# Kernel tuning notes

Measured on AMD Instinct MI355X. Metric: run time of the kernel, lower is better.

Reference implementation:

```python
import jax, jax.numpy as jnp
import numpy as np

N = 100000   # nodes
E = 1600000  # directed edges
HID = 64


def gat_conv(x, src, dst, W, a_src, a_dst, b, heads, out_ch):
    """PyG-style GATConv (add_self_loops=True, negative_slope=0.2, concat)."""
    n = x.shape[0]
    h = (x @ W).reshape(n, heads, out_ch)              # [N,H,C]
    loop = jnp.arange(n, dtype=src.dtype)
    s = jnp.concatenate([src, loop])                   # self loops appended
    d = jnp.concatenate([dst, loop])
    alpha_src = jnp.sum(h * a_src, axis=-1)            # [N,H]
    alpha_dst = jnp.sum(h * a_dst, axis=-1)            # [N,H]
    alpha = jax.nn.leaky_relu(alpha_src[s] + alpha_dst[d], 0.2)  # [E+N,H]
    # segment softmax over incoming edges of each destination node
    amax = jax.ops.segment_max(alpha, d, num_segments=n)
    alpha = jnp.exp(alpha - amax[d])
    asum = jax.ops.segment_sum(alpha, d, num_segments=n)
    alpha = alpha / (asum[d] + 1e-16)
    msg = h[s] * alpha[:, :, None]                     # [E+N,H,C]
    out = jax.ops.segment_sum(msg, d, num_segments=n)  # [N,H,C]
    return out.reshape(n, heads * out_ch) + b


def setup_inputs() -> dict:
    key = jax.random.key(0)
    ks = jax.random.split(key, 22)
    rn = lambda k, shp, s=0.1: (jax.random.normal(k, shp, jnp.float32) * s)
    inp = {
        "x": jax.random.normal(ks[0], (N, 2), jnp.float32),
        "edge_index": jax.random.randint(ks[1], (2, E), 0, N, dtype=jnp.int32),
        "edge_attr": jax.random.normal(ks[2], (E, 2), jnp.float32),
        # node encoder
        "enc_W": rn(ks[3], (2, HID)), "enc_b": rn(ks[4], (HID,)),
        # gat1: heads=4, out=16
        "g1_W": rn(ks[5], (HID, HID)), "g1_as": rn(ks[6], (4, 16)),
        "g1_ad": rn(ks[7], (4, 16)), "g1_b": rn(ks[8], (HID,)),
        # gat2: heads=1, out=64
        "g2_W": rn(ks[9], (HID, HID)), "g2_as": rn(ks[10], (1, HID)),
        "g2_ad": rn(ks[11], (1, HID)), "g2_b": rn(ks[12], (HID,)),
        # node head
        "no_W1": rn(ks[13], (HID, HID)), "no_b1": rn(ks[14], (HID,)),
        "no_W2": rn(ks[15], (HID, 2)), "no_b2": rn(ks[16], (2,)),
        # edge head: in = 2*HID + 2 = 130
        "eo_W1": rn(ks[17], (2 * HID + 2, HID)), "eo_b1": rn(ks[18], (HID,)),
        "eo_W2": rn(ks[19], (HID, 1)), "eo_b2": rn(ks[20], (1,)),
    }
    return inp


def reference(x, edge_index, edge_attr, enc_W, enc_b,
              g1_W, g1_as, g1_ad, g1_b,
              g2_W, g2_as, g2_ad, g2_b,
              no_W1, no_b1, no_W2, no_b2,
              eo_W1, eo_b1, eo_W2, eo_b2):
    src, dst = edge_index[0], edge_index[1]
    h = x @ enc_W + enc_b                                    # node encoder (dropout = eval identity)
    h = jax.nn.elu(gat_conv(h, src, dst, g1_W, g1_as, g1_ad, g1_b, 4, 16))
    h = gat_conv(h, src, dst, g2_W, g2_as, g2_ad, g2_b, 1, HID)
    e_in = jnp.concatenate([h[src], h[dst], edge_attr], axis=-1)  # [E,130]
    node_pred = jnp.tanh(jax.nn.leaky_relu(h @ no_W1 + no_b1, 0.01) @ no_W2 + no_b2)
    edge_pred = jnp.tanh(jax.nn.leaky_relu(e_in @ eo_W1 + eo_b1, 0.01) @ eo_W2 + eo_b2)[:, 0]
    return edge_pred, node_pred
```

## Files before the change

kernel.cpp:

```cpp
#include <hip/hip_runtime.h>
#include <hip/hip_fp16.h>
#include <math.h>


typedef _Float16 half8_t __attribute__((ext_vector_type(8)));
typedef _Float16 half4_t __attribute__((ext_vector_type(4)));
typedef float floatx4 __attribute__((ext_vector_type(4)));

__global__ void k_scatter(const int* __restrict__ src, const int* __restrict__ dst,
                          int E, int NB, int cap, int* cursor,
                          unsigned int* __restrict__ ebuf,
                          const float* __restrict__ encW, const float* __restrict__ encb,
                          const float* __restrict__ g1W, float* __restrict__ Mc){
  __shared__ int hist[800];
  __shared__ int base[800];
  int t = threadIdx.x;
  if (blockIdx.x == 0 && t < 64){
    float m0 = 0.f, m1 = 0.f, cc = 0.f;
    for (int k = 0; k < 64; ++k){
      float g = g1W[k * 64 + t];
      m0 = fmaf(encW[k], g, m0);
      m1 = fmaf(encW[64 + k], g, m1);
      cc = fmaf(encb[k], g, cc);
    }
    Mc[t] = m0; Mc[64 + t] = m1; Mc[128 + t] = cc;
  }
  for (int i = t; i < NB; i += 256) hist[i] = 0;
  __syncthreads();
  int cbase = blockIdx.x * 2048;
  int sv[8], bk[8], dl[8], rk[8];
  #pragma unroll
  for (int i = 0; i < 8; ++i){
    int e = cbase + i * 256 + t;
    if (e < E){
      int d = dst[e];
      sv[i] = src[e]; bk[i] = d >> 7; dl[i] = d & 127;
      rk[i] = atomicAdd(&hist[bk[i]], 1);
    } else bk[i] = -1;
  }
  __syncthreads();
  for (int i = t; i < NB; i += 256){
    int c = hist[i];
    base[i] = (c > 0) ? (i * cap + atomicAdd(&cursor[i], c)) : 0;
  }
  __syncthreads();
  #pragma unroll
  for (int i = 0; i < 8; ++i){
    if (bk[i] >= 0){
      int p = base[bk[i]] + rk[i];
      if (p < (bk[i] + 1) * cap)
        ebuf[p] = (unsigned)sv[i] | ((unsigned)dl[i] << 17);
    }
  }
}

__global__ void k_bucket_build(const int* __restrict__ cursor, int cap, int N,
                               unsigned int* ebuf, int* __restrict__ rstart,
                               int* __restrict__ rend,
                               const float* __restrict__ as4,
                               const float* __restrict__ ad4,
                               half4_t* __restrict__ palpha4){
  __shared__ unsigned int ent[2700];
  __shared__ unsigned short rank[2700];
  __shared__ int cnts[128];
  __shared__ int aux[128];
  int b = blockIdx.x, t = threadIdx.x;
  int base = b * cap;
  int cnt = cursor[b];
  if (cnt > cap) cnt = cap;
  for (int i = t; i < cnt; i += 256) ent[i] = ebuf[base + i];
  if (t < 128) cnts[t] = 0;
  __syncthreads();
  for (int i = t; i < cnt; i += 256)
    rank[i] = (unsigned short)atomicAdd(&cnts[ent[i] >> 17], 1);
  __syncthreads();
  int v = 0;
  if (t < 128){ v = cnts[t]; aux[t] = v; }
  __syncthreads();
  for (int off = 1; off < 128; off <<= 1){
    int x = 0;
    if (t < 128 && t >= off) x = aux[t - off];
    __syncthreads();
    if (t < 128) aux[t] += x;
    __syncthreads();
  }
  if (t < 128){
    int incl = aux[t];
    int node = (b << 7) + t;
    if (node < N){ rstart[node] = base + incl - v; rend[node] = base + incl; }
    cnts[t] = incl - v;
  }
  __syncthreads();
  for (int i = t; i < cnt; i += 256){
    unsigned int en = ent[i];
    int dl = en >> 17;
    int s = en & 0x1FFFFu;
    int pos = cnts[dl] + (int)rank[i];
    ebuf[base + pos] = en;
    int d = (b << 7) + dl;
    float4 sv = ((const float4*)as4)[s];
    float4 dv = ((const float4*)ad4)[d];
    float a0 = sv.x + dv.x, a1 = sv.y + dv.y, a2 = sv.z + dv.z, a3 = sv.w + dv.w;
    a0 = a0 > 0.f ? a0 : 0.2f * a0;
    a1 = a1 > 0.f ? a1 : 0.2f * a1;
    a2 = a2 > 0.f ? a2 : 0.2f * a2;
    a3 = a3 > 0.f ? a3 : 0.2f * a3;
    half4_t pv = {(_Float16)__expf(a0), (_Float16)__expf(a1),
                  (_Float16)__expf(a2), (_Float16)__expf(a3)};
    palpha4[base + pos] = pv;
  }
}

__global__ void k_palpha1(const int* __restrict__ cursor, int cap,
                          const unsigned int* __restrict__ ebuf,
                          const float* __restrict__ as, const float* __restrict__ ad,
                          _Float16* __restrict__ palpha1){
  int blk = blockIdx.x;
  int b = blk >> 2, part = blk & 3;
  int base = b * cap;
  int cnt = cursor[b];
  if (cnt > cap) cnt = cap;
  for (int i = part * 256 + threadIdx.x; i < cnt; i += 1024){
    unsigned int en = ebuf[base + i];
    int s = en & 0x1FFFFu;
    int d = (b << 7) + (en >> 17);
    float a = as[s] + ad[d];
    a = a > 0.f ? a : 0.2f * a;
    palpha1[base + i] = (_Float16)__expf(a);
  }
}

__global__ void k_fuse1(const float* __restrict__ x, const float* __restrict__ Mc,
                        const float* __restrict__ a_s, const float* __restrict__ a_d,
                        __half* __restrict__ hw, float* __restrict__ alpha_s,
                        float* __restrict__ alpha_d, int n){
  int idx = blockIdx.x * blockDim.x + threadIdx.x;
  if (idx >= n * 64) return;
  int node = idx >> 6, j = idx & 63;
  float acc = fmaf(x[node * 2 + 0], Mc[j], fmaf(x[node * 2 + 1], Mc[64 + j], Mc[128 + j]));
  hw[idx] = __float2half(acc);
  float ps = acc * a_s[j];
  float pd = acc * a_d[j];
  #pragma unroll
  for (int off = 1; off < 16; off <<= 1){
    ps += __shfl_xor(ps, off);
    pd += __shfl_xor(pd, off);
  }
  if ((j & 15) == 0){
    int h = j >> 4;
    alpha_s[node * 4 + h] = ps;
    alpha_d[node * 4 + h] = pd;
  }
}

__global__ __launch_bounds__(256) void k_hw_mfma(
    const __half* __restrict__ hin, const float* __restrict__ W,
    const float* __restrict__ a_s, const float* __restrict__ a_d,
    __half* __restrict__ hw, float* __restrict__ alpha_s,
    float* __restrict__ alpha_d, int n){
  __shared__ float redS[4][16];
  __shared__ float redD[4][16];
  int t = threadIdx.x;
  int lane = t & 63, wave = t >> 6;
  int l15 = lane & 15, quad = lane >> 4;
  int ch = wave * 16 + l15;
  half8_t b0, b1;
  #pragma unroll
  for (int j = 0; j < 8; ++j){
    b0[j] = (_Float16)W[(quad * 8 + j) * 64 + ch];
    b1[j] = (_Float16)W[(quad * 8 + j + 32) * 64 + ch];
  }
  float asv = a_s[ch], adv = a_d[ch];
  int base = blockIdx.x * 64;
  for (int it = 0; it < 4; ++it){
    int tb = base + it * 16;
    if (tb >= n) break;
    int arn = tb + l15; if (arn >= n) arn = n - 1;
    const __half* arow = hin + (size_t)arn * 64 + quad * 8;
    half8_t a0 = *(const half8_t*)arow;
    half8_t a1 = *(const half8_t*)(arow + 32);
    floatx4 acc = {0.f, 0.f, 0.f, 0.f};
    acc = __builtin_amdgcn_mfma_f32_16x16x32_f16(a0, b0, acc, 0, 0, 0);
    acc = __builtin_amdgcn_mfma_f32_16x16x32_f16(a1, b1, acc, 0, 0, 0);
    float ps[4], pd[4];
    #pragma unroll
    for (int r = 0; r < 4; ++r){
      int node = tb + quad * 4 + r;
      if (node < n) hw[(size_t)node * 64 + ch] = __float2half(acc[r]);
      ps[r] = acc[r] * asv;
      pd[r] = acc[r] * adv;
      #pragma unroll
      for (int off = 1; off < 16; off <<= 1){
        ps[r] += __shfl_xor(ps[r], off);
        pd[r] += __shfl_xor(pd[r], off);
      }
    }
    if (l15 == 0){
      #pragma unroll
      for (int r = 0; r < 4; ++r){
        redS[wave][quad * 4 + r] = ps[r];
        redD[wave][quad * 4 + r] = pd[r];
      }
    }
    __syncthreads();
    if (t < 16 && tb + t < n){
      alpha_s[tb + t] = redS[0][t] + redS[1][t] + redS[2][t] + redS[3][t];
      alpha_d[tb + t] = redD[0][t] + redD[1][t] + redD[2][t] + redD[3][t];
    }
    __syncthreads();
  }
}

template<int H, bool ELU_ACT>
__global__ void k_agg(const __half* __restrict__ hw, const _Float16* __restrict__ palpha,
                      const float* __restrict__ alpha_s, const float* __restrict__ alpha_d,
                      const int* __restrict__ rstart, const int* __restrict__ rend,
                      const unsigned int* __restrict__ ebuf,
                      const float* __restrict__ bias, __half* __restrict__ hout, int n){
  int node = (blockIdx.x * blockDim.x + threadIdx.x) >> 6;
  int lane = threadIdx.x & 63;
  int g = lane >> 3, jj = lane & 7;
  if (node >= n) return;
  int hidx = (jj * H) >> 3;
  int start = rstart[node], end = rend[node];
  float acc[8] = {0.f,0.f,0.f,0.f,0.f,0.f,0.f,0.f};
  float psum = 0.f;
  if (g == 0){
    float a = alpha_s[node * H + hidx] + alpha_d[node * H + hidx];
    a = a > 0.f ? a : 0.2f * a;
    float p = __expf(a);
    psum = p;
    float4 rv = *(const float4*)(hw + (size_t)node * 64 + jj * 8);
    const __half2* hp = (const __half2*)&rv;
    #pragma unroll
    for (int k = 0; k < 4; ++k){
      float2 f = __half22float2(hp[k]);
      acc[2 * k] = p * f.x; acc[2 * k + 1] = p * f.y;
    }
  }
  int i = start + g;
  for (; i + 8 < end; i += 16){
    unsigned int e0 = ebuf[i], e1 = ebuf[i + 8];
    int s0 = e0 & 0x1FFFF, s1 = e1 & 0x1FFFF;
    float p0 = (float)palpha[(size_t)i * H + hidx];
    float p1 = (float)palpha[(size_t)(i + 8) * H + hidx];
    float4 r0 = *(const float4*)(hw + (size_t)s0 * 64 + jj * 8);
    float4 r1 = *(const float4*)(hw + (size_t)s1 * 64 + jj * 8);
    const __half2* h0 = (const __half2*)&r0;
    const __half2* h1 = (const __half2*)&r1;
    psum += p0 + p1;
    #pragma unroll
    for (int k = 0; k < 4; ++k){
      float2 f0 = __half22float2(h0[k]);
      float2 f1 = __half22float2(h1[k]);
      acc[2 * k]     = fmaf(p0, f0.x, fmaf(p1, f1.x, acc[2 * k]));
      acc[2 * k + 1] = fmaf(p0, f0.y, fmaf(p1, f1.y, acc[2 * k + 1]));
    }
  }
  if (i < end){
    unsigned int en = ebuf[i];
    int s = en & 0x1FFFF;
    float p = (float)palpha[(size_t)i * H + hidx];
    float4 rv = *(const float4*)(hw + (size_t)s * 64 + jj * 8);
    const __half2* hp = (const __half2*)&rv;
    psum += p;
    #pragma unroll
    for (int k = 0; k < 4; ++k){
      float2 f = __half22float2(hp[k]);
      acc[2 * k]     = fmaf(p, f.x, acc[2 * k]);
      acc[2 * k + 1] = fmaf(p, f.y, acc[2 * k + 1]);
    }
  }
  #pragma unroll
  for (int off = 8; off < 64; off <<= 1){
    psum += __shfl_xor(psum, off);
    #pragma unroll
    for (int k = 0; k < 8; ++k) acc[k] += __shfl_xor(acc[k], off);
  }
  if (g == 0){
    float inv = 1.f / (psum + 1e-16f);
    float4 bv0 = ((const float4*)bias)[2 * jj];
    float4 bv1 = ((const float4*)bias)[2 * jj + 1];
    float o[8];
    o[0] = fmaf(acc[0], inv, bv0.x); o[1] = fmaf(acc[1], inv, bv0.y);
    o[2] = fmaf(acc[2], inv, bv0.z); o[3] = fmaf(acc[3], inv, bv0.w);
    o[4] = fmaf(acc[4], inv, bv1.x); o[5] = fmaf(acc[5], inv, bv1.y);
    o[6] = fmaf(acc[6], inv, bv1.z); o[7] = fmaf(acc[7], inv, bv1.w);
    if (ELU_ACT){
      #pragma unroll
      for (int k = 0; k < 8; ++k) o[k] = o[k] > 0.f ? o[k] : (__expf(o[k]) - 1.f);
    }
    half8_t hv;
    #pragma unroll
    for (int k = 0; k < 8; ++k) hv[k] = (_Float16)o[k];
    *(half8_t*)(hout + (size_t)node * 64 + jj * 8) = hv;
  }
}

__global__ __launch_bounds__(256) void k_heads_mfma(
    const __half* __restrict__ h, const float* __restrict__ eoW1,
    const float* __restrict__ noW1, const float* __restrict__ nob1,
    const float* __restrict__ noW2, const float* __restrict__ nob2,
    __half* __restrict__ P1, __half* __restrict__ P2,
    float* __restrict__ outN, int n){
  __shared__ float redP[4][16][2];
  int t = threadIdx.x;
  int lane = t & 63, wave = t >> 6;
  int l15 = lane & 15, quad = lane >> 4;
  int ch = wave * 16 + l15;
  half8_t bP1a, bP1b, bP2a, bP2b, bNa, bNb;
  #pragma unroll
  for (int j = 0; j < 8; ++j){
    int k0 = quad * 8 + j, k1 = k0 + 32;
    bP1a[j] = (_Float16)eoW1[k0 * 64 + ch];
    bP1b[j] = (_Float16)eoW1[k1 * 64 + ch];
    bP2a[j] = (_Float16)eoW1[(k0 + 64) * 64 + ch];
    bP2b[j] = (_Float16)eoW1[(k1 + 64) * 64 + ch];
    bNa[j]  = (_Float16)noW1[k0 * 64 + ch];
    bNb[j]  = (_Float16)noW1[k1 * 64 + ch];
  }
  float b1v = nob1[ch];
  float w20 = noW2[ch * 2 + 0], w21 = noW2[ch * 2 + 1];
  float b20 = nob2[0], b21 = nob2[1];
  int base = blockIdx.x * 64;
  for (int it = 0; it < 4; ++it){
    int tb = base + it * 16;
    if (tb >= n) break;
    int arn = tb + l15; if (arn >= n) arn = n - 1;
    const __half* arow = h + (size_t)arn * 64 + quad * 8;
    half8_t a0 = *(const half8_t*)arow;
    half8_t a1 = *(const half8_t*)(arow + 32);
    floatx4 ac1 = {0.f,0.f,0.f,0.f}, ac2 = {0.f,0.f,0.f,0.f}, acN = {0.f,0.f,0.f,0.f};
    ac1 = __builtin_amdgcn_mfma_f32_16x16x32_f16(a0, bP1a, ac1, 0, 0, 0);
    ac1 = __builtin_amdgcn_mfma_f32_16x16x32_f16(a1, bP1b, ac1, 0, 0, 0);
    ac2 = __builtin_amdgcn_mfma_f32_16x16x32_f16(a0, bP2a, ac2, 0, 0, 0);
    ac2 = __builtin_amdgcn_mfma_f32_16x16x32_f16(a1, bP2b, ac2, 0, 0, 0);
    acN = __builtin_amdgcn_mfma_f32_16x16x32_f16(a0, bNa, acN, 0, 0, 0);
    acN = __builtin_amdgcn_mfma_f32_16x16x32_f16(a1, bNb, acN, 0, 0, 0);
    float p0[4], p1[4];
    #pragma unroll
    for (int r = 0; r < 4; ++r){
      int node = tb + quad * 4 + r;
      if (node < n){
        P1[(size_t)node * 64 + ch] = __float2half(ac1[r]);
        P2[(size_t)node * 64 + ch] = __float2half(ac2[r]);
      }
      float v = acN[r] + b1v;
      v = v > 0.f ? v : 0.01f * v;
      p0[r] = v * w20;
      p1[r] = v * w21;
      #pragma unroll
      for (int off = 1; off < 16; off <<= 1){
        p0[r] += __shfl_xor(p0[r], off);
        p1[r] += __shfl_xor(p1[r], off);
      }
    }
    if (l15 == 0){
      #pragma unroll
      for (int r = 0; r < 4; ++r){
        redP[wave][quad * 4 + r][0] = p0[r];
        redP[wave][quad * 4 + r][1] = p1[r];
      }
    }
    __syncthreads();
    if (t < 16 && tb + t < n){
      float s0 = redP[0][t][0] + redP[1][t][0] + redP[2][t][0] + redP[3][t][0];
      float s1 = redP[0][t][1] + redP[1][t][1] + redP[2][t][1] + redP[3][t][1];
      outN[(size_t)(tb + t) * 2 + 0] = tanhf(s0 + b20);
      outN[(size_t)(tb + t) * 2 + 1] = tanhf(s1 + b21);
    }
    __syncthreads();
  }
}

__global__ void k_edge_head(const __half* __restrict__ P1h, const __half* __restrict__ P2h,
                            const int* __restrict__ src, const int* __restrict__ dst,
                            const float* __restrict__ eattr, const float* __restrict__ eoW1,
                            const float* __restrict__ b1, const float* __restrict__ W2,
                            const float* __restrict__ b2, float* __restrict__ out, int E){
  int lane = threadIdx.x & 63;
  int jj = lane & 7, q = lane >> 3;
  int wid = (blockIdx.x * blockDim.x + threadIdx.x) >> 6;
  int nw = (gridDim.x * blockDim.x) >> 6;

  const float4* rAq = (const float4*)(eoW1 + 8192);
  const float4* rBq = (const float4*)(eoW1 + 8256);
  const float4* b1q = (const float4*)b1;
  const float4* w2q = (const float4*)W2;
  float4 tA0 = rAq[2 * jj], tA1 = rAq[2 * jj + 1];
  float4 tB0 = rBq[2 * jj], tB1 = rBq[2 * jj + 1];
  float4 tb0 = b1q[2 * jj], tb1 = b1q[2 * jj + 1];
  float4 tw0 = w2q[2 * jj], tw1 = w2q[2 * jj + 1];
  float ra[8] = {tA0.x, tA0.y, tA0.z, tA0.w, tA1.x, tA1.y, tA1.z, tA1.w};
  float rb[8] = {tB0.x, tB0.y, tB0.z, tB0.w, tB1.x, tB1.y, tB1.z, tB1.w};
  float bb[8] = {tb0.x, tb0.y, tb0.z, tb0.w, tb1.x, tb1.y, tb1.z, tb1.w};
  float w2[8] = {tw0.x, tw0.y, tw0.z, tw0.w, tw1.x, tw1.y, tw1.z, tw1.w};
  float b2v = b2[0];

  const float4* P1q = (const float4*)P1h;
  const float4* P2q = (const float4*)P2h;
  const float2* eav = (const float2*)eattr;

  int groups = (E + 15) >> 4;
  for (int g = wid; g < groups; g += nw){
    int e0 = g * 16 + q, e1 = e0 + 8;
    bool act0 = (e0 < E), act1 = (e1 < E);
    float p0 = 0.f, p1 = 0.f;
    if (act0){
      int s = src[e0], d = dst[e0];
      float2 ea = eav[e0];
      float4 g1 = P1q[(size_t)s * 8 + jj];
      float4 g2 = P2q[(size_t)d * 8 + jj];
      const __half2* h1 = (const __half2*)&g1;
      const __half2* h2 = (const __half2*)&g2;
      #pragma unroll
      for (int k = 0; k < 4; ++k){
        float2 u = __half22float2(h1[k]);
        float2 w = __half22float2(h2[k]);
        float ta = u.x + w.x + bb[2 * k];
        float tb = u.y + w.y + bb[2 * k + 1];
        ta = fmaf(ea.x, ra[2 * k], fmaf(ea.y, rb[2 * k], ta));
        tb = fmaf(ea.x, ra[2 * k + 1], fmaf(ea.y, rb[2 * k + 1], tb));
        ta = ta > 0.f ? ta : 0.01f * ta;
        tb = tb > 0.f ? tb : 0.01f * tb;
        p0 = fmaf(ta, w2[2 * k], fmaf(tb, w2[2 * k + 1], p0));
      }
    }
    if (act1){
      int s = src[e1], d = dst[e1];
      float2 ea = eav[e1];
      float4 g1 = P1q[(size_t)s * 8 + jj];
      float4 g2 = P2q[(size_t)d * 8 + jj];
      const __half2* h1 = (const __half2*)&g1;
      const __half2* h2 = (const __half2*)&g2;
      #pragma unroll
      for (int k = 0; k < 4; ++k){
        float2 u = __half22float2(h1[k]);
        float2 w = __half22float2(h2[k]);
        float ta = u.x + w.x + bb[2 * k];
        float tb = u.y + w.y + bb[2 * k + 1];
        ta = fmaf(ea.x, ra[2 * k], fmaf(ea.y, rb[2 * k], ta));
        tb = fmaf(ea.x, ra[2 * k + 1], fmaf(ea.y, rb[2 * k + 1], tb));
        ta = ta > 0.f ? ta : 0.01f * ta;
        tb = tb > 0.f ? tb : 0.01f * tb;
        p1 = fmaf(ta, w2[2 * k], fmaf(tb, w2[2 * k + 1], p1));
      }
    }
    #pragma unroll
    for (int off = 1; off < 8; off <<= 1){
      p0 += __shfl_xor(p0, off);
      p1 += __shfl_xor(p1, off);
    }
    if (jj == 0){
      if (act0) out[e0] = tanhf(p0 + b2v);
      if (act1) out[e1] = tanhf(p1 + b2v);
    }
  }
}

extern "C" void kernel_launch(void* const* d_in, const int* in_sizes, int n_in,
                              void* d_out, int out_size, void* d_ws, size_t ws_size,
                              hipStream_t stream){
  const float* x    = (const float*)d_in[0];
  const int*   eidx = (const int*)  d_in[1];
  const float* ea   = (const float*)d_in[2];
  const float* encW = (const float*)d_in[3];
  const float* encb = (const float*)d_in[4];
  const float* g1W  = (const float*)d_in[5];
  const float* g1as = (const float*)d_in[6];
  const float* g1ad = (const float*)d_in[7];
  const float* g1b  = (const float*)d_in[8];
  const float* g2W  = (const float*)d_in[9];
  const float* g2as = (const float*)d_in[10];
  const float* g2ad = (const float*)d_in[11];
  const float* g2b  = (const float*)d_in[12];
  const float* noW1 = (const float*)d_in[13];
  const float* nob1 = (const float*)d_in[14];
  const float* noW2 = (const float*)d_in[15];
  const float* nob2 = (const float*)d_in[16];
  const float* eoW1 = (const float*)d_in[17];
  const float* eob1 = (const float*)d_in[18];
  const float* eoW2 = (const float*)d_in[19];
  const float* eob2 = (const float*)d_in[20];

  const int N = in_sizes[0] / 2;
  const int E = in_sizes[1] / 2;
  const int* src = eidx;
  const int* dst = eidx + E;

  const int NB = (N + 127) >> 7;
  int avg = (E + NB - 1) / NB;
  int cap = avg + avg / 4 + 64;
  if (cap > 2700) cap = 2700;

  char* ws = (char*)d_ws;
  size_t off = 0;
  auto alloc = [&](size_t bytes) -> void* {
    void* p = ws + off;
    off = (off + bytes + 255) & ~(size_t)255;
    return p;
  };
  __half* bufA  = (__half*)alloc((size_t)N * 64 * 2);
  __half* bufH  = (__half*)alloc((size_t)N * 64 * 2);
  __half* P1h   = (__half*)alloc((size_t)N * 64 * 2);
  __half* P2h   = (__half*)alloc((size_t)N * 64 * 2);
  float*  as    = (float*) alloc((size_t)N * 4 * 4);
  float*  ad    = (float*) alloc((size_t)N * 4 * 4);
  int* rstart   = (int*)   alloc((size_t)N * 4);
  int* rend     = (int*)   alloc((size_t)N * 4);
  unsigned int* ebuf = (unsigned int*)alloc((size_t)NB * cap * 4);
  _Float16* palphaB = (_Float16*)alloc((size_t)NB * cap * 8);
  int* cursor   = (int*)   alloc((size_t)NB * 4);
  float* Mc     = (float*) alloc(192 * 4);

  hipMemsetAsync(cursor, 0, (size_t)NB * 4, stream);
  k_scatter<<<(E + 2047) / 2048, 256, 0, stream>>>(src, dst, E, NB, cap, cursor, ebuf,
                                                   encW, encb, g1W, Mc);
  k_fuse1<<<(N * 64 + 255) / 256, 256, 0, stream>>>(x, Mc, g1as, g1ad, bufH, as, ad, N);
  k_bucket_build<<<NB, 256, 0, stream>>>(cursor, cap, N, ebuf, rstart, rend,
                                         as, ad, (half4_t*)palphaB);
  k_agg<4, true><<<(N + 3) / 4, 256, 0, stream>>>(bufH, palphaB, as, ad,
                                                  rstart, rend, ebuf, g1b, bufA, N);
  k_hw_mfma<<<(N + 63) / 64, 256, 0, stream>>>(bufA, g2W, g2as, g2ad, bufH, as, ad, N);
  k_palpha1<<<NB * 4, 256, 0, stream>>>(cursor, cap, ebuf, as, ad, palphaB);
  k_agg<1, false><<<(N + 3) / 4, 256, 0, stream>>>(bufH, palphaB, as, ad,
                                                   rstart, rend, ebuf, g2b, bufA, N);
  float* out = (float*)d_out;
  k_heads_mfma<<<(N + 63) / 64, 256, 0, stream>>>(bufA, eoW1, noW1, nob1, noW2, nob2,
                                                  P1h, P2h, out + E, N);
  k_edge_head<<<2048, 256, 0, stream>>>(P1h, P2h, src, dst, ea,
                                        eoW1, eob1, eoW2, eob2, out, E);
}
```

Measured before the change: 387.4 us.

## Fuse node encoder into scatter kernel and inline layer-2 attention in aggregation

Merges the first-layer projection (k_fuse1) into the edge scatter kernel via a grid-stride loop, with every block recomputing the small folded weight matrix into shared memory. It also drops the k_palpha1 pass by computing layer-2 edge attention weights on the fly inside the aggregation kernel from alpha_s/alpha_d. The goal is fewer launches and no write-then-read of the per-edge palpha buffer. In exchange each block repeats the 64x64 fold, and each edge in layer 2 needs an extra gather of alpha_s plus an exp.

New measurement: 378.2 us. 2.4% less time.

```diff
diff --git a/kernel.cpp b/kernel.cpp
--- a/kernel.cpp
+++ b/kernel.cpp
@@ -7,15 +7,20 @@
 typedef _Float16 half4_t __attribute__((ext_vector_type(4)));
 typedef float floatx4 __attribute__((ext_vector_type(4)));
 
-__global__ void k_scatter(const int* __restrict__ src, const int* __restrict__ dst,
-                          int E, int NB, int cap, int* cursor,
-                          unsigned int* __restrict__ ebuf,
-                          const float* __restrict__ encW, const float* __restrict__ encb,
-                          const float* __restrict__ g1W, float* __restrict__ Mc){
+__global__ void k_scatter_fuse(const int* __restrict__ src, const int* __restrict__ dst,
+                               int E, int NB, int cap, int* cursor,
+                               unsigned int* __restrict__ ebuf,
+                               const float* __restrict__ x,
+                               const float* __restrict__ encW, const float* __restrict__ encb,
+                               const float* __restrict__ g1W,
+                               const float* __restrict__ g1as, const float* __restrict__ g1ad,
+                               __half* __restrict__ hw, float* __restrict__ alpha_s,
+                               float* __restrict__ alpha_d, int n){
   __shared__ int hist[800];
   __shared__ int base[800];
+  __shared__ float McS[192];
   int t = threadIdx.x;
-  if (blockIdx.x == 0 && t < 64){
+  if (t < 64){
     float m0 = 0.f, m1 = 0.f, cc = 0.f;
     for (int k = 0; k < 64; ++k){
       float g = g1W[k * 64 + t];
@@ -23,7 +28,7 @@
       m1 = fmaf(encW[64 + k], g, m1);
       cc = fmaf(encb[k], g, cc);
     }
-    Mc[t] = m0; Mc[64 + t] = m1; Mc[128 + t] = cc;
+    McS[t] = m0; McS[64 + t] = m1; McS[128 + t] = cc;
   }
   for (int i = t; i < NB; i += 256) hist[i] = 0;
   __syncthreads();
@@ -50,6 +55,26 @@
       int p = base[bk[i]] + rk[i];
       if (p < (bk[i] + 1) * cap)
         ebuf[p] = (unsigned)sv[i] | ((unsigned)dl[i] << 17);
+    }
+  }
+  int total = n * 64;
+  int lane = t & 63;
+  for (int idx = blockIdx.x * 256 + t; idx < total; idx += gridDim.x * 256){
+    int node = idx >> 6;
+    float acc = fmaf(x[node * 2 + 0], McS[lane],
+                fmaf(x[node * 2 + 1], McS[64 + lane], McS[128 + lane]));
+    hw[idx] = __float2half(acc);
+    float ps = acc * g1as[lane];
+    float pd = acc * g1ad[lane];
+    #pragma unroll
+    for (int off = 1; off < 16; off <<= 1){
+      ps += __shfl_xor(ps, off);
+      pd += __shfl_xor(pd, off);
+    }
+    if ((lane & 15) == 0){
+      int h = lane >> 4;
+      alpha_s[node * 4 + h] = ps;
+      alpha_d[node * 4 + h] = pd;
     }
   }
 }
@@ -111,48 +136,6 @@
   }
 }
 
-__global__ void k_palpha1(const int* __restrict__ cursor, int cap,
-                          const unsigned int* __restrict__ ebuf,
-                          const float* __restrict__ as, const float* __restrict__ ad,
-                          _Float16* __restrict__ palpha1){
-  int blk = blockIdx.x;
-  int b = blk >> 2, part = blk & 3;
-  int base = b * cap;
-  int cnt = cursor[b];
-  if (cnt > cap) cnt = cap;
-  for (int i = part * 256 + threadIdx.x; i < cnt; i += 1024){
-    unsigned int en = ebuf[base + i];
-    int s = en & 0x1FFFFu;
-    int d = (b << 7) + (en >> 17);
-    float a = as[s] + ad[d];
-    a = a > 0.f ? a : 0.2f * a;
-    palpha1[base + i] = (_Float16)__expf(a);
-  }
-}
-
-__global__ void k_fuse1(const float* __restrict__ x, const float* __restrict__ Mc,
-                        const float* __restrict__ a_s, const float* __restrict__ a_d,
-                        __half* __restrict__ hw, float* __restrict__ alpha_s,
-                        float* __restrict__ alpha_d, int n){
-  int idx = blockIdx.x * blockDim.x + threadIdx.x;
-  if (idx >= n * 64) return;
-  int node = idx >> 6, j = idx & 63;
-  float acc = fmaf(x[node * 2 + 0], Mc[j], fmaf(x[node * 2 + 1], Mc[64 + j], Mc[128 + j]));
-  hw[idx] = __float2half(acc);
-  float ps = acc * a_s[j];
-  float pd = acc * a_d[j];
-  #pragma unroll
-  for (int off = 1; off < 16; off <<= 1){
-    ps += __shfl_xor(ps, off);
-    pd += __shfl_xor(pd, off);
-  }
-  if ((j & 15) == 0){
-    int h = j >> 4;
-    alpha_s[node * 4 + h] = ps;
-    alpha_d[node * 4 + h] = pd;
-  }
-}
-
 __global__ __launch_bounds__(256) void k_hw_mfma(
     const __half* __restrict__ hin, const float* __restrict__ W,
     const float* __restrict__ a_s, const float* __restrict__ a_d,
@@ -211,7 +194,7 @@
   }
 }
 
-template<int H, bool ELU_ACT>
+template<int H, bool ELU_ACT, bool INLINE_A>
 __global__ void k_agg(const __half* __restrict__ hw, const _Float16* __restrict__ palpha,
                       const float* __restrict__ alpha_s, const float* __restrict__ alpha_d,
                       const int* __restrict__ rstart, const int* __restrict__ rend,
@@ -223,6 +206,7 @@
   if (node >= n) return;
   int hidx = (jj * H) >> 3;
   int start = rstart[node], end = rend[node];
+  float adn = INLINE_A ? alpha_d[node] : 0.f;
   float acc[8] = {0.f,0.f,0.f,0.f,0.f,0.f,0.f,0.f};
   float psum = 0.f;
   if (g == 0){
@@ -242,8 +226,17 @@
   for (; i + 8 < end; i += 16){
     unsigned int e0 = ebuf[i], e1 = ebuf[i + 8];
     int s0 = e0 & 0x1FFFF, s1 = e1 & 0x1FFFF;
-    float p0 = (float)palpha[(size_t)i * H + hidx];
-    float p1 = (float)palpha[(size_t)(i + 8) * H + hidx];
+    float p0, p1;
+    if (INLINE_A){
+      float a0 = alpha_s[s0] + adn;
+      float a1 = alpha_s[s1] + adn;
+      a0 = a0 > 0.f ? a0 : 0.2f * a0;
+      a1 = a1 > 0.f ? a1 : 0.2f * a1;
+      p0 = __expf(a0); p1 = __expf(a1);
+    } else {
+      p0 = (float)palpha[(size_t)i * H + hidx];
+      p1 = (float)palpha[(size_t)(i + 8) * H + hidx];
+    }
     float4 r0 = *(const float4*)(hw + (size_t)s0 * 64 + jj * 8);
     float4 r1 = *(const float4*)(hw + (size_t)s1 * 64 + jj * 8);
     const __half2* h0 = (const __half2*)&r0;
@@ -260,7 +253,14 @@
   if (i < end){
     unsigned int en = ebuf[i];
     int s = en & 0x1FFFF;
-    float p = (float)palpha[(size_t)i * H + hidx];
+    float p;
+    if (INLINE_A){
+      float a = alpha_s[s] + adn;
+      a = a > 0.f ? a : 0.2f * a;
+      p = __expf(a);
+    } else {
+      p = (float)palpha[(size_t)i * H + hidx];
+    }
     float4 rv = *(const float4*)(hw + (size_t)s * 64 + jj * 8);
     const __half2* hp = (const __half2*)&rv;
     psum += p;
@@ -511,20 +511,18 @@
   unsigned int* ebuf = (unsigned int*)alloc((size_t)NB * cap * 4);
   _Float16* palphaB = (_Float16*)alloc((size_t)NB * cap * 8);
   int* cursor   = (int*)   alloc((size_t)NB * 4);
-  float* Mc     = (float*) alloc(192 * 4);
 
   hipMemsetAsync(cursor, 0, (size_t)NB * 4, stream);
-  k_scatter<<<(E + 2047) / 2048, 256, 0, stream>>>(src, dst, E, NB, cap, cursor, ebuf,
-                                                   encW, encb, g1W, Mc);
-  k_fuse1<<<(N * 64 + 255) / 256, 256, 0, stream>>>(x, Mc, g1as, g1ad, bufH, as, ad, N);
+  k_scatter_fuse<<<(E + 2047) / 2048, 256, 0, stream>>>(
+      src, dst, E, NB, cap, cursor, ebuf,
+      x, encW, encb, g1W, g1as, g1ad, bufH, as, ad, N);
   k_bucket_build<<<NB, 256, 0, stream>>>(cursor, cap, N, ebuf, rstart, rend,
                                          as, ad, (half4_t*)palphaB);
-  k_agg<4, true><<<(N + 3) / 4, 256, 0, stream>>>(bufH, palphaB, as, ad,
-                                                  rstart, rend, ebuf, g1b, bufA, N);
+  k_agg<4, true, false><<<(N + 3) / 4, 256, 0, stream>>>(bufH, palphaB, as, ad,
+                                                         rstart, rend, ebuf, g1b, bufA, N);
   k_hw_mfma<<<(N + 63) / 64, 256, 0, stream>>>(bufA, g2W, g2as, g2ad, bufH, as, ad, N);
-  k_palpha1<<<NB * 4, 256, 0, stream>>>(cursor, cap, ebuf, as, ad, palphaB);
-  k_agg<1, false><<<(N + 3) / 4, 256, 0, stream>>>(bufH, palphaB, as, ad,
-                                                   rstart, rend, ebuf, g2b, bufA, N);
+  k_agg<1, false, true><<<(N + 3) / 4, 256, 0, stream>>>(bufH, palphaB, as, ad,
+                                                         rstart, rend, ebuf, g2b, bufA, N);
   float* out = (float*)d_out;
   k_heads_mfma<<<(N + 63) / 64, 256, 0, stream>>>(bufA, eoW1, noW1, nob1, noW2, nob2,
                                                   P1h, P2h, out + E, N);
```
